# Kernel tuning notes

Hardware: AMD Instinct MI355X
Metric: run time of the kernel (lower is better)

## Reference

```python
import jax, jax.numpy as jnp
import numpy as np

B, S, D = 2, 2048, 2048
H, KVH, HD = 8, 1, 256          # query heads, kv heads, head_dim (GQA: n_rep = H // KVH)
ROPE_THETA = 10000.0
NEG_INF = -1e9


def setup_inputs() -> dict:
    key = jax.random.key(0)
    k1, k2, k3, k4, k5 = jax.random.split(key, 5)
    hidden_states = jax.random.normal(k1, (B, S, D), dtype=jnp.float32)
    # additive causal mask: 0 where allowed, -inf where masked, shape (B,1,S,S)
    causal = jnp.tril(jnp.ones((S, S), dtype=bool))
    attention_mask = jnp.where(causal, 0.0, NEG_INF).astype(jnp.float32)
    attention_mask = jnp.broadcast_to(attention_mask[None, None], (B, 1, S, S))
    position_ids = jnp.broadcast_to(jnp.arange(S, dtype=jnp.int32)[None, :], (B, S))
    sc = 0.02
    Wq = jax.random.normal(k2, (H * HD, D), dtype=jnp.float32) * sc   # torch Linear weight layout [out,in]
    Wk = jax.random.normal(k3, (KVH * HD, D), dtype=jnp.float32) * sc
    Wv = jax.random.normal(k4, (KVH * HD, D), dtype=jnp.float32) * sc
    Wo = jax.random.normal(k5, (D, H * HD), dtype=jnp.float32) * sc
    return {"hidden_states": hidden_states, "attention_mask": attention_mask,
            "position_ids": position_ids, "Wq": Wq, "Wk": Wk, "Wv": Wv, "Wo": Wo}


def _rotate_half(x):
    x1, x2 = jnp.split(x, 2, axis=-1)
    return jnp.concatenate((-x2, x1), axis=-1)


def _rope_cos_sin(position_ids):
    inv_freq = 1.0 / (ROPE_THETA ** (jnp.arange(0, HD, 2, dtype=jnp.float32) / HD))  # [HD/2]
    freqs = position_ids.astype(jnp.float32)[:, :, None] * inv_freq[None, None, :]   # [B,S,HD/2]
    emb = jnp.concatenate((freqs, freqs), axis=-1)                                   # [B,S,HD]
    return jnp.cos(emb)[:, None], jnp.sin(emb)[:, None]                              # [B,1,S,HD]


def reference(hidden_states, attention_mask, position_ids, Wq, Wk, Wv, Wo):
    q = (hidden_states @ Wq.T).reshape(B, S, H, HD).transpose(0, 2, 1, 3)     # [B,H,S,HD]
    k = (hidden_states @ Wk.T).reshape(B, S, KVH, HD).transpose(0, 2, 1, 3)   # [B,KVH,S,HD]
    v = (hidden_states @ Wv.T).reshape(B, S, KVH, HD).transpose(0, 2, 1, 3)
    cos, sin = _rope_cos_sin(position_ids)
    q = q * cos + _rotate_half(q) * sin
    k = k * cos + _rotate_half(k) * sin
    n_rep = H // KVH
    k = jnp.repeat(k, n_rep, axis=1)                                          # repeat_kv -> [B,H,S,HD]
    v = jnp.repeat(v, n_rep, axis=1)
    scores = jnp.einsum('bhqd,bhkd->bhqk', q, k) / jnp.sqrt(jnp.float32(HD))
    scores = scores + attention_mask
    attn = jax.nn.softmax(scores, axis=-1)                                    # dropout p=0 (eval)
    ctx = jnp.einsum('bhqk,bhkd->bhqd', attn, v)
    ctx = ctx.transpose(0, 2, 1, 3).reshape(B, S, H * HD)
    out = ctx @ Wo.T
    return out, attn
```

## Files before the change

kernel.cpp:

```cpp
#include <hip/hip_runtime.h>
#include <hip/hip_bf16.h>
#include <math.h>

typedef __bf16 bf16_t;
typedef __bf16 bf16x8 __attribute__((ext_vector_type(8)));
typedef float  f32x4  __attribute__((ext_vector_type(4)));

#define DEV __device__ __forceinline__

constexpr int B_   = 2;
constexpr int S_   = 2048;
constexpr int D_   = 2048;
constexpr int H_   = 8;
constexpr int HD_  = 256;
constexpr int NQKV_ = H_ * HD_ + 2 * HD_;
constexpr int TOK_ = B_ * S_;

#if defined(__has_builtin)
#if __has_builtin(__builtin_amdgcn_global_load_lds)
#define HAS_GLLDS 1
#endif
#endif

DEV void stage16(const bf16_t* g, bf16_t* l) {
#ifdef HAS_GLLDS
  __builtin_amdgcn_global_load_lds((const __attribute__((address_space(1))) void*)g,
                                   (__attribute__((address_space(3))) void*)l, 16, 0, 0);
#else
  *(bf16x8*)l = *(const bf16x8*)g;
#endif
}

__global__ void cast_inputs(const float* __restrict__ hs, const float* __restrict__ wq,
                            const float* __restrict__ wk, const float* __restrict__ wv,
                            const float* __restrict__ wo,
                            bf16_t* __restrict__ Xb, bf16_t* __restrict__ Wqkvb,
                            bf16_t* __restrict__ Wob) {
  const size_t i = (size_t)blockIdx.x * blockDim.x + threadIdx.x;
  const size_t NHS = (size_t)TOK_ * D_;
  const size_t NWQ = (size_t)H_ * HD_ * D_;
  const size_t NWK = (size_t)HD_ * D_;
  if (i < NHS) Xb[i] = (bf16_t)hs[i];
  if (i < NWQ) { Wqkvb[i] = (bf16_t)wq[i]; Wob[i] = (bf16_t)wo[i]; }
  if (i < NWK) { Wqkvb[NWQ + i] = (bf16_t)wk[i]; Wqkvb[NWQ + NWK + i] = (bf16_t)wv[i]; }
}

template <bool CBF16>
__global__ __launch_bounds__(256, 2)
void gemm_bt(const bf16_t* __restrict__ Ab, const bf16_t* __restrict__ Bg,
             void* __restrict__ Cv, int K, int lda, int ldb, int ldc)
{
  const int bn = blockIdx.x, bm = blockIdx.y;
  const int m0 = bm * 128, n0 = bn * 128;

  __shared__ __align__(16) bf16_t Asm[128 * 32];
  __shared__ __align__(16) bf16_t Bsm[128 * 32];

  const int tid  = threadIdx.x;
  const int l    = tid & 63;
  const int w    = tid >> 6;
  const int wm   = (w >> 1) * 64;
  const int wn   = (w & 1) * 64;
  const int lrow = l & 15;
  const int quad = l >> 4;

  f32x4 acc[4][4] = {};

  for (int k0 = 0; k0 < K; k0 += 32) {
    __syncthreads();
    #pragma unroll
    for (int c = 0; c < 2; ++c) {
      int chunk = c * 256 + tid;
      int row = chunk >> 2, col = (chunk & 3) << 3;
      stage16(Ab + (size_t)(m0 + row) * lda + (k0 + col), &Asm[row * 32 + col]);
      stage16(Bg + (size_t)(n0 + row) * ldb + (k0 + col), &Bsm[row * 32 + col]);
    }
    __syncthreads();

    bf16x8 af[4], bfr[4];
    #pragma unroll
    for (int i = 0; i < 4; ++i)
      af[i] = *(const bf16x8*)&Asm[(wm + i * 16 + lrow) * 32 + quad * 8];
    #pragma unroll
    for (int j = 0; j < 4; ++j)
      bfr[j] = *(const bf16x8*)&Bsm[(wn + j * 16 + lrow) * 32 + quad * 8];
    #pragma unroll
    for (int i = 0; i < 4; ++i)
      #pragma unroll
      for (int j = 0; j < 4; ++j)
        acc[i][j] = __builtin_amdgcn_mfma_f32_16x16x32_bf16(af[i], bfr[j], acc[i][j], 0, 0, 0);
  }

  #pragma unroll
  for (int i = 0; i < 4; ++i) {
    int row = wm + i * 16 + quad * 4;
    #pragma unroll
    for (int j = 0; j < 4; ++j) {
      int col = n0 + wn + j * 16 + lrow;
      #pragma unroll
      for (int r = 0; r < 4; ++r) {
        if (CBF16) ((bf16_t*)Cv)[(size_t)(m0 + row + r) * ldc + col] = (bf16_t)acc[i][j][r];
        else       ((float*) Cv)[(size_t)(m0 + row + r) * ldc + col] = acc[i][j][r];
      }
    }
  }
}

__global__ void rope_kernel(const bf16_t* __restrict__ qkv, const int* __restrict__ pos_ids,
                            bf16_t* __restrict__ Qh, bf16_t* __restrict__ Kb,
                            bf16_t* __restrict__ Vt)
{
  const int t = blockIdx.x;
  const int b = t >> 11, s = t & (S_ - 1);
  const int tid = threadIdx.x;
  const int pd = tid & 127, half = tid >> 7;
  const float pos = (float)pos_ids[t];
  const float expo = (float)(2 * pd) * (1.0f / 256.0f);
  const float invf = 1.0f / powf(10000.0f, expo);
  const float ang = pos * invf;
  const float c = cosf(ang), sn = sinf(ang);
  const bf16_t* base = qkv + (size_t)t * NQKV_;
  const int other = half ? tid - 128 : tid + 128;
  const float sgn = half ? 1.0f : -1.0f;
  #pragma unroll
  for (int h = 0; h < H_; ++h) {
    float x = (float)base[h * HD_ + tid];
    float xo = (float)base[h * HD_ + other];
    Qh[((size_t)(b * H_ + h) * S_ + s) * HD_ + tid] = (bf16_t)(x * c + sgn * xo * sn);
  }
  {
    float x = (float)base[D_ + tid], xo = (float)base[D_ + other];
    Kb[(size_t)t * HD_ + tid] = (bf16_t)(x * c + sgn * xo * sn);
  }
  Vt[((size_t)b * HD_ + tid) * S_ + s] = base[D_ + HD_ + tid];
}

constexpr int PSTR = 136;

DEV void compute_S(const bf16_t* __restrict__ Kg, bf16_t* __restrict__ KV,
                   const bf16x8 aq[8], f32x4 accS[8],
                   int kb, int tid, int lrow, int quad)
{
  #pragma unroll
  for (int half = 0; half < 2; ++half) {
    __syncthreads();
    #pragma unroll
    for (int it = 0; it < 8; ++it) {
      int s = it * 256 + tid;
      int c = s >> 6, key = s & 63;
      stage16(Kg + (size_t)(kb * 128 + half * 64 + key) * HD_ + c * 8, KV + s * 8);
    }
    __syncthreads();
    #pragma unroll
    for (int kk = 0; kk < 8; ++kk) {
      bf16x8 bk[4];
      #pragma unroll
      for (int j = 0; j < 4; ++j)
        bk[j] = *(const bf16x8*)&KV[((kk * 4 + quad) * 64 + j * 16 + lrow) * 8];
      #pragma unroll
      for (int j = 0; j < 4; ++j)
        accS[half * 4 + j] =
            __builtin_amdgcn_mfma_f32_16x16x32_bf16(aq[kk], bk[j], accS[half * 4 + j], 0, 0, 0);
    }
  }
}

__global__ __launch_bounds__(256, 2)
void flash_attn(const bf16_t* __restrict__ Qh, const bf16_t* __restrict__ Kbp,
                const bf16_t* __restrict__ Vt, bf16_t* __restrict__ Ctx,
                float* __restrict__ lsum)
{
  const int idx = blockIdx.x;
  int z, qb;
  if (idx < 256) { z = idx & 15; qb = idx >> 4; }
  else           { int j = idx - 256; z = j & 15; qb = 31 - (j >> 4); }
  const int b = z >> 3, h = z & 7;
  const int q0 = qb * 64;
  const bf16_t* Qg = Qh + ((size_t)z * S_ + q0) * HD_;
  const bf16_t* Kg = Kbp + (size_t)b * S_ * HD_;
  const bf16_t* Vg = Vt + (size_t)b * HD_ * S_;

  __shared__ __align__(16) bf16_t KV[64 * 256];
  __shared__ __align__(16) bf16_t Pst[4 * 16 * PSTR];

  const int tid = threadIdx.x;
  const int w = tid >> 6, l = tid & 63;
  const int lrow = l & 15, quad = l >> 4;
  const int nkb = (qb >> 1) + 1;
  const float scale = 0.0625f;

  bf16x8 aq[8];
  const bf16_t* qrow = Qg + (size_t)(w * 16 + lrow) * HD_ + quad * 8;
  #pragma unroll
  for (int kk = 0; kk < 8; ++kk) aq[kk] = *(const bf16x8*)(qrow + kk * 32);

  const int rowg0 = q0 + w * 16 + quad * 4;
  float lp[4] = {0.f, 0.f, 0.f, 0.f};
  f32x4 accO[16] = {};
  bf16_t* pw = &Pst[w * 16 * PSTR];

  for (int kb = 0; kb < nkb; ++kb) {
    f32x4 accS[8] = {};
    compute_S(Kg, KV, aq, accS, kb, tid, lrow, quad);

    #pragma unroll
    for (int r = 0; r < 4; ++r) {
      #pragma unroll
      for (int j = 0; j < 8; ++j) {
        int col = kb * 128 + j * 16 + lrow;
        float p = (col <= rowg0 + r) ? __expf(accS[j][r] * scale) : 0.f;
        lp[r] += p;
        pw[(quad * 4 + r) * PSTR + j * 16 + lrow] = (bf16_t)p;
      }
    }
    bf16x8 ap[4];
    #pragma unroll
    for (int kk2 = 0; kk2 < 4; ++kk2)
      ap[kk2] = *(const bf16x8*)&pw[lrow * PSTR + kk2 * 32 + quad * 8];

    #pragma unroll
    for (int half = 0; half < 2; ++half) {
      __syncthreads();
      #pragma unroll
      for (int it = 0; it < 8; ++it) {
        int s = it * 256 + tid;
        int c2 = s >> 8, d = s & 255;
        stage16(Vg + (size_t)d * S_ + kb * 128 + half * 64 + c2 * 8, KV + s * 8);
      }
      __syncthreads();
      #pragma unroll
      for (int kkl = 0; kkl < 2; ++kkl) {
        #pragma unroll
        for (int j2 = 0; j2 < 16; ++j2) {
          bf16x8 bv = *(const bf16x8*)&KV[((kkl * 4 + quad) * 256 + j2 * 16 + lrow) * 8];
          accO[j2] = __builtin_amdgcn_mfma_f32_16x16x32_bf16(ap[half * 2 + kkl], bv, accO[j2], 0, 0, 0);
        }
      }
    }
  }

  #pragma unroll
  for (int r = 0; r < 4; ++r) {
    #pragma unroll
    for (int o = 1; o < 16; o <<= 1) lp[r] += __shfl_xor(lp[r], o, 64);
  }
  float inv[4];
  #pragma unroll
  for (int r = 0; r < 4; ++r) inv[r] = 1.0f / lp[r];

  #pragma unroll
  for (int j2 = 0; j2 < 16; ++j2) {
    #pragma unroll
    for (int r = 0; r < 4; ++r) {
      int rowq = q0 + w * 16 + quad * 4 + r;
      Ctx[((size_t)b * S_ + rowq) * D_ + h * HD_ + j2 * 16 + lrow] = (bf16_t)(accO[j2][r] * inv[r]);
    }
  }
  if (lrow == 0) {
    #pragma unroll
    for (int r = 0; r < 4; ++r) lsum[(size_t)z * S_ + rowg0 + r] = lp[r];
  }
}

__global__ __launch_bounds__(256, 2)
void p_writer(const bf16_t* __restrict__ Qh, const bf16_t* __restrict__ Kbp,
              const float* __restrict__ lsum, float* __restrict__ attn)
{
  const int bn = blockIdx.x, bm = blockIdx.y, z = blockIdx.z;
  const int m0 = bm * 128, n0 = bn * 128;
  float* Pg = attn + (size_t)z * S_ * S_;
  const int tid = threadIdx.x;

  if (bn > bm) {
    #pragma unroll
    for (int it = 0; it < 16; ++it) {
      int idx = it * 256 + tid;
      int row = idx >> 5, c4 = idx & 31;
      *(f32x4*)&Pg[(size_t)(m0 + row) * S_ + n0 + c4 * 4] = f32x4{0.f, 0.f, 0.f, 0.f};
    }
    return;
  }

  const bf16_t* Ab = Qh + (size_t)z * S_ * HD_;
  const bf16_t* Bg = Kbp + (size_t)(z >> 3) * S_ * HD_;

  __shared__ __align__(16) bf16_t Asm[128 * 32];
  __shared__ __align__(16) bf16_t Bsm[128 * 32];

  const int l    = tid & 63;
  const int w    = tid >> 6;
  const int wm   = (w >> 1) * 64;
  const int wn   = (w & 1) * 64;
  const int lrow = l & 15;
  const int quad = l >> 4;

  f32x4 acc[4][4] = {};

  for (int k0 = 0; k0 < HD_; k0 += 32) {
    __syncthreads();
    #pragma unroll
    for (int c = 0; c < 2; ++c) {
      int chunk = c * 256 + tid;
      int row = chunk >> 2, col = (chunk & 3) << 3;
      stage16(Ab + (size_t)(m0 + row) * HD_ + (k0 + col), &Asm[row * 32 + col]);
      stage16(Bg + (size_t)(n0 + row) * HD_ + (k0 + col), &Bsm[row * 32 + col]);
    }
    __syncthreads();

    bf16x8 af[4], bfr[4];
    #pragma unroll
    for (int i = 0; i < 4; ++i)
      af[i] = *(const bf16x8*)&Asm[(wm + i * 16 + lrow) * 32 + quad * 8];
    #pragma unroll
    for (int j = 0; j < 4; ++j)
      bfr[j] = *(const bf16x8*)&Bsm[(wn + j * 16 + lrow) * 32 + quad * 8];
    #pragma unroll
    for (int i = 0; i < 4; ++i)
      #pragma unroll
      for (int j = 0; j < 4; ++j)
        acc[i][j] = __builtin_amdgcn_mfma_f32_16x16x32_bf16(af[i], bfr[j], acc[i][j], 0, 0, 0);
  }

  const float scale = 0.0625f;
  #pragma unroll
  for (int i = 0; i < 4; ++i) {
    int row = m0 + wm + i * 16 + quad * 4;
    #pragma unroll
    for (int r = 0; r < 4; ++r) {
      const float il = 1.0f / lsum[(size_t)z * S_ + row + r];
      float* prow = &Pg[(size_t)(row + r) * S_];
      #pragma unroll
      for (int j = 0; j < 4; ++j) {
        int col = n0 + wn + j * 16 + lrow;
        prow[col] = (col <= row + r) ? __expf(acc[i][j][r] * scale) * il : 0.f;
      }
    }
  }
}

extern "C" void kernel_launch(void* const* d_in, const int* in_sizes, int n_in,
                              void* d_out, int out_size, void* d_ws, size_t ws_size,
                              hipStream_t stream)
{
  const float* hs  = (const float*)d_in[0];
  const int*   pos = (const int*)d_in[2];
  const float* wq  = (const float*)d_in[3];
  const float* wk  = (const float*)d_in[4];
  const float* wv  = (const float*)d_in[5];
  const float* wo  = (const float*)d_in[6];

  float* out  = (float*)d_out;
  float* attn = out + (size_t)TOK_ * D_;

  char* ws = (char*)d_ws;
  bf16_t* Xb    = (bf16_t*)(ws);
  bf16_t* Wqkvb = (bf16_t*)(ws + 16777216);
  bf16_t* Wob   = (bf16_t*)(ws + 27262976);
  bf16_t* QKVb  = (bf16_t*)(ws + 35651584);
  bf16_t* Qh    = (bf16_t*)(ws + 56623104);
  bf16_t* Kb    = (bf16_t*)(ws + 73400320);
  bf16_t* Vt    = (bf16_t*)(ws + 75497472);
  bf16_t* Ctx   = (bf16_t*)(ws + 77594624);
  float*  lsum  = (float* )(ws + 94371840);

  cast_inputs<<<(TOK_ * D_) / 256, 256, 0, stream>>>(hs, wq, wk, wv, wo, Xb, Wqkvb, Wob);
  gemm_bt<true><<<dim3(NQKV_ / 128, TOK_ / 128), 256, 0, stream>>>(
      Xb, Wqkvb, QKVb, D_, D_, D_, NQKV_);
  rope_kernel<<<TOK_, 256, 0, stream>>>(QKVb, pos, Qh, Kb, Vt);
  flash_attn<<<512, 256, 0, stream>>>(Qh, Kb, Vt, Ctx, lsum);
  p_writer<<<dim3(S_ / 128, S_ / 128, B_ * H_), 256, 0, stream>>>(Qh, Kb, lsum, attn);
  gemm_bt<false><<<dim3(D_ / 128, TOK_ / 128), 256, 0, stream>>>(
      Ctx, Wob, out, D_, D_, D_, D_);
}
```

Before: 665.7 us.

## Pre-tile K and V into LDS-ready chunks and vectorize RoPE

RoPE now processes 8 elements per thread with vector loads and stores, and writes K both row-major and in a 64-key chunked layout that matches the LDS staging order. A new v_trans kernel transposes V into the same chunked layout, so flash attention stages each chunk with fully contiguous 16-byte loads instead of strided gathers. s_setprio is raised around the MFMA loops. The cost is an extra kernel launch, an extra K copy in the workspace, and a different RoPE frequency computation using exp2f.

```diff
diff --git a/kernel.cpp b/kernel.cpp
--- a/kernel.cpp
+++ b/kernel.cpp
@@ -15,6 +15,7 @@
 constexpr int HD_  = 256;
 constexpr int NQKV_ = H_ * HD_ + 2 * HD_;
 constexpr int TOK_ = B_ * S_;
+constexpr int CHK_ = 64 * HD_;
 
 #if defined(__has_builtin)
 #if __has_builtin(__builtin_amdgcn_global_load_lds)
@@ -108,49 +109,89 @@
 
 __global__ void rope_kernel(const bf16_t* __restrict__ qkv, const int* __restrict__ pos_ids,
                             bf16_t* __restrict__ Qh, bf16_t* __restrict__ Kb,
-                            bf16_t* __restrict__ Vt)
+                            bf16_t* __restrict__ K2)
 {
   const int t = blockIdx.x;
   const int b = t >> 11, s = t & (S_ - 1);
   const int tid = threadIdx.x;
-  const int pd = tid & 127, half = tid >> 7;
+  const int h = tid >> 5, c = tid & 31;
   const float pos = (float)pos_ids[t];
-  const float expo = (float)(2 * pd) * (1.0f / 256.0f);
-  const float invf = 1.0f / powf(10000.0f, expo);
-  const float ang = pos * invf;
-  const float c = cosf(ang), sn = sinf(ang);
+  const int pdbase = (c & 15) * 8;
+  float cs[8], sn[8];
+  #pragma unroll
+  for (int j = 0; j < 8; ++j) {
+    float invf = exp2f((float)(pdbase + j) * -0.103810253f);
+    float ang = pos * invf;
+    cs[j] = cosf(ang); sn[j] = sinf(ang);
+  }
+  const float sgn = (c < 16) ? -1.0f : 1.0f;
   const bf16_t* base = qkv + (size_t)t * NQKV_;
-  const int other = half ? tid - 128 : tid + 128;
-  const float sgn = half ? 1.0f : -1.0f;
-  #pragma unroll
-  for (int h = 0; h < H_; ++h) {
-    float x = (float)base[h * HD_ + tid];
-    float xo = (float)base[h * HD_ + other];
-    Qh[((size_t)(b * H_ + h) * S_ + s) * HD_ + tid] = (bf16_t)(x * c + sgn * xo * sn);
-  }
+
   {
-    float x = (float)base[D_ + tid], xo = (float)base[D_ + other];
-    Kb[(size_t)t * HD_ + tid] = (bf16_t)(x * c + sgn * xo * sn);
-  }
-  Vt[((size_t)b * HD_ + tid) * S_ + s] = base[D_ + HD_ + tid];
+    bf16x8 x  = *(const bf16x8*)(base + h * HD_ + c * 8);
+    bf16x8 xo = *(const bf16x8*)(base + h * HD_ + (c ^ 16) * 8);
+    bf16x8 o;
+    #pragma unroll
+    for (int j = 0; j < 8; ++j)
+      o[j] = (bf16_t)((float)x[j] * cs[j] + sgn * (float)xo[j] * sn[j]);
+    *(bf16x8*)(Qh + ((size_t)(b * H_ + h) * S_ + s) * HD_ + c * 8) = o;
+  }
+  if (h == 0) {
+    bf16x8 x  = *(const bf16x8*)(base + D_ + c * 8);
+    bf16x8 xo = *(const bf16x8*)(base + D_ + (c ^ 16) * 8);
+    bf16x8 o;
+    #pragma unroll
+    for (int j = 0; j < 8; ++j)
+      o[j] = (bf16_t)((float)x[j] * cs[j] + sgn * (float)xo[j] * sn[j]);
+    *(bf16x8*)(Kb + (size_t)t * HD_ + c * 8) = o;
+    const int chunk = s >> 6, key = s & 63;
+    *(bf16x8*)(K2 + (size_t)(b * 32 + chunk) * CHK_ + c * 512 + key * 8) = o;
+  }
+}
+
+__global__ void v_trans(const bf16_t* __restrict__ qkv, bf16_t* __restrict__ V2)
+{
+  const int blk = blockIdx.x;
+  const int s0 = (blk & 31) * 64;
+  const int b = blk >> 5;
+  const int tid = threadIdx.x;
+  __shared__ bf16_t L[64][264];
+  #pragma unroll
+  for (int it = 0; it < 8; ++it) {
+    int gi = it * 256 + tid;
+    int r = gi >> 5, cc = gi & 31;
+    *(bf16x8*)&L[r][cc * 8] =
+        *(const bf16x8*)(qkv + ((size_t)b * S_ + s0 + r) * NQKV_ + (D_ + HD_) + cc * 8);
+  }
+  __syncthreads();
+  bf16_t* out = V2 + (size_t)blk * CHK_;
+  #pragma unroll
+  for (int it = 0; it < 8; ++it) {
+    int G = it * 256 + tid;
+    bf16x8 o;
+    #pragma unroll
+    for (int j = 0; j < 8; ++j) o[j] = L[it * 8 + j][tid];
+    *(bf16x8*)(out + (size_t)G * 8) = o;
+  }
 }
 
 constexpr int PSTR = 136;
 
-DEV void compute_S(const bf16_t* __restrict__ Kg, bf16_t* __restrict__ KV,
+DEV void compute_S(const bf16_t* __restrict__ K2g, bf16_t* __restrict__ KV,
                    const bf16x8 aq[8], f32x4 accS[8],
                    int kb, int tid, int lrow, int quad)
 {
   #pragma unroll
   for (int half = 0; half < 2; ++half) {
     __syncthreads();
+    const bf16_t* src = K2g + (size_t)(kb * 2 + half) * CHK_;
     #pragma unroll
     for (int it = 0; it < 8; ++it) {
       int s = it * 256 + tid;
-      int c = s >> 6, key = s & 63;
-      stage16(Kg + (size_t)(kb * 128 + half * 64 + key) * HD_ + c * 8, KV + s * 8);
-    }
-    __syncthreads();
+      stage16(src + (size_t)s * 8, KV + s * 8);
+    }
+    __syncthreads();
+    __builtin_amdgcn_s_setprio(1);
     #pragma unroll
     for (int kk = 0; kk < 8; ++kk) {
       bf16x8 bk[4];
@@ -162,12 +203,13 @@
         accS[half * 4 + j] =
             __builtin_amdgcn_mfma_f32_16x16x32_bf16(aq[kk], bk[j], accS[half * 4 + j], 0, 0, 0);
     }
+    __builtin_amdgcn_s_setprio(0);
   }
 }
 
 __global__ __launch_bounds__(256, 2)
-void flash_attn(const bf16_t* __restrict__ Qh, const bf16_t* __restrict__ Kbp,
-                const bf16_t* __restrict__ Vt, bf16_t* __restrict__ Ctx,
+void flash_attn(const bf16_t* __restrict__ Qh, const bf16_t* __restrict__ K2,
+                const bf16_t* __restrict__ V2, bf16_t* __restrict__ Ctx,
                 float* __restrict__ lsum)
 {
   const int idx = blockIdx.x;
@@ -176,9 +218,9 @@
   else           { int j = idx - 256; z = j & 15; qb = 31 - (j >> 4); }
   const int b = z >> 3, h = z & 7;
   const int q0 = qb * 64;
-  const bf16_t* Qg = Qh + ((size_t)z * S_ + q0) * HD_;
-  const bf16_t* Kg = Kbp + (size_t)b * S_ * HD_;
-  const bf16_t* Vg = Vt + (size_t)b * HD_ * S_;
+  const bf16_t* Qg  = Qh + ((size_t)z * S_ + q0) * HD_;
+  const bf16_t* K2g = K2 + (size_t)b * 32 * CHK_;
+  const bf16_t* V2g = V2 + (size_t)b * 32 * CHK_;
 
   __shared__ __align__(16) bf16_t KV[64 * 256];
   __shared__ __align__(16) bf16_t Pst[4 * 16 * PSTR];
@@ -201,7 +243,7 @@
 
   for (int kb = 0; kb < nkb; ++kb) {
     f32x4 accS[8] = {};
-    compute_S(Kg, KV, aq, accS, kb, tid, lrow, quad);
+    compute_S(K2g, KV, aq, accS, kb, tid, lrow, quad);
 
     #pragma unroll
     for (int r = 0; r < 4; ++r) {
@@ -221,13 +263,14 @@
     #pragma unroll
     for (int half = 0; half < 2; ++half) {
       __syncthreads();
+      const bf16_t* src = V2g + (size_t)(kb * 2 + half) * CHK_;
       #pragma unroll
       for (int it = 0; it < 8; ++it) {
         int s = it * 256 + tid;
-        int c2 = s >> 8, d = s & 255;
-        stage16(Vg + (size_t)d * S_ + kb * 128 + half * 64 + c2 * 8, KV + s * 8);
+        stage16(src + (size_t)s * 8, KV + s * 8);
       }
       __syncthreads();
+      __builtin_amdgcn_s_setprio(1);
       #pragma unroll
       for (int kkl = 0; kkl < 2; ++kkl) {
         #pragma unroll
@@ -236,6 +279,7 @@
           accO[j2] = __builtin_amdgcn_mfma_f32_16x16x32_bf16(ap[half * 2 + kkl], bv, accO[j2], 0, 0, 0);
         }
       }
+      __builtin_amdgcn_s_setprio(0);
     }
   }
 
@@ -359,15 +403,17 @@
   bf16_t* QKVb  = (bf16_t*)(ws + 35651584);
   bf16_t* Qh    = (bf16_t*)(ws + 56623104);
   bf16_t* Kb    = (bf16_t*)(ws + 73400320);
-  bf16_t* Vt    = (bf16_t*)(ws + 75497472);
+  bf16_t* V2    = (bf16_t*)(ws + 75497472);
   bf16_t* Ctx   = (bf16_t*)(ws + 77594624);
   float*  lsum  = (float* )(ws + 94371840);
+  bf16_t* K2    = (bf16_t*)(ws + 94502912);
 
   cast_inputs<<<(TOK_ * D_) / 256, 256, 0, stream>>>(hs, wq, wk, wv, wo, Xb, Wqkvb, Wob);
   gemm_bt<true><<<dim3(NQKV_ / 128, TOK_ / 128), 256, 0, stream>>>(
       Xb, Wqkvb, QKVb, D_, D_, D_, NQKV_);
-  rope_kernel<<<TOK_, 256, 0, stream>>>(QKVb, pos, Qh, Kb, Vt);
-  flash_attn<<<512, 256, 0, stream>>>(Qh, Kb, Vt, Ctx, lsum);
+  rope_kernel<<<TOK_, 256, 0, stream>>>(QKVb, pos, Qh, Kb, K2);
+  v_trans<<<B_ * 32, 256, 0, stream>>>(QKVb, V2);
+  flash_attn<<<512, 256, 0, stream>>>(Qh, K2, V2, Ctx, lsum);
   p_writer<<<dim3(S_ / 128, S_ / 128, B_ * H_), 256, 0, stream>>>(Qh, Kb, lsum, attn);
   gemm_bt<false><<<dim3(D_ / 128, TOK_ / 128), 256, 0, stream>>>(
       Ctx, Wob, out, D_, D_, D_, D_);
```

New measurement: 622.1 us. -6.6%, faster.
